# Kernel tuning notes

Measured on AMD Instinct MI355X. Metric: run time of the kernel, lower is better.

Reference implementation:

```python
import jax, jax.numpy as jnp
import numpy as np

N_NODES = 50000
N_EDGES = 800000
NODE_DIM = 8
EDGE_DIM = 3
HIDDEN = 256
EMBED = 256
HEADS = 4
HEAD_DIM = HIDDEN // HEADS
LAYERS = 3
NUM_GRAPHS = 64
NEG_SLOPE = 0.2


def layer_norm(x, g, b, eps=1e-5):
    mu = jnp.mean(x, axis=-1, keepdims=True)
    var = jnp.var(x, axis=-1, keepdims=True)
    return (x - mu) * jax.lax.rsqrt(var + eps) * g + b


def setup_inputs() -> dict:
    key = jax.random.key(0)
    ks = jax.random.split(key, 20)
    s = lambda d: 1.0 / np.sqrt(d)
    inp = {
        "x": jax.random.normal(ks[0], (N_NODES, NODE_DIM), jnp.float32),
        "edge_index": jax.random.randint(ks[1], (2, N_EDGES), 0, N_NODES, jnp.int64),
        "edge_attr": jax.random.normal(ks[2], (N_EDGES, EDGE_DIM), jnp.float32),
        "batch": jnp.sort(jax.random.randint(ks[3], (N_NODES,), 0, NUM_GRAPHS, jnp.int64)),
        # input projection + LayerNorm
        "W_in": jax.random.normal(ks[4], (NODE_DIM, HIDDEN), jnp.float32) * s(NODE_DIM),
        "b_in": jnp.zeros((HIDDEN,), jnp.float32),
        "ln_in_g": jnp.ones((HIDDEN,), jnp.float32),
        "ln_in_b": jnp.zeros((HIDDEN,), jnp.float32),
        # stacked GAT layer params [LAYERS, ...]
        "W_gat": jax.random.normal(ks[5], (LAYERS, HIDDEN, HIDDEN), jnp.float32) * s(HIDDEN),
        "b_gat": jnp.zeros((LAYERS, HIDDEN), jnp.float32),
        "W_e": jax.random.normal(ks[6], (LAYERS, EDGE_DIM, HIDDEN), jnp.float32) * s(EDGE_DIM),
        "a_src": jax.random.normal(ks[7], (LAYERS, HEADS, HEAD_DIM), jnp.float32) * s(HEAD_DIM),
        "a_dst": jax.random.normal(ks[8], (LAYERS, HEADS, HEAD_DIM), jnp.float32) * s(HEAD_DIM),
        "a_edge": jax.random.normal(ks[9], (LAYERS, HEADS, HEAD_DIM), jnp.float32) * s(HEAD_DIM),
        # output projection + LayerNorm
        "W_out": jax.random.normal(ks[10], (EMBED, EMBED), jnp.float32) * s(EMBED),
        "b_out": jnp.zeros((EMBED,), jnp.float32),
        "ln_out_g": jnp.ones((EMBED,), jnp.float32),
        "ln_out_b": jnp.zeros((EMBED,), jnp.float32),
    }
    return inp


def gat_layer(h, src, dst, edge_attr, W, b, We, a_s, a_d, a_e):
    N = h.shape[0]
    hp = (h @ W + b).reshape(N, HEADS, HEAD_DIM)                 # [N,H,D]
    ep = (edge_attr @ We).reshape(-1, HEADS, HEAD_DIM)           # [E,H,D]
    hs = hp[src]                                                 # [E,H,D] gather
    hd = hp[dst]
    logit = (hs * a_s).sum(-1) + (hd * a_d).sum(-1) + (ep * a_e).sum(-1)  # [E,H]
    logit = jax.nn.leaky_relu(logit, NEG_SLOPE)
    # segment softmax over incoming edges per destination node
    m = jax.ops.segment_max(logit, dst, num_segments=N)          # [N,H]
    m = jnp.where(jnp.isfinite(m), m, 0.0)
    ex = jnp.exp(logit - m[dst])
    denom = jax.ops.segment_sum(ex, dst, num_segments=N)         # [N,H]
    alpha = ex / jnp.maximum(denom[dst], 1e-16)                  # [E,H]
    msg = hs * alpha[:, :, None]                                 # [E,H,D]
    out = jax.ops.segment_sum(msg, dst, num_segments=N).reshape(N, HIDDEN)
    return jax.nn.elu(out + h)                                   # residual + activation


def reference(x, edge_index, edge_attr, batch, W_in, b_in, ln_in_g, ln_in_b,
              W_gat, b_gat, W_e, a_src, a_dst, a_edge,
              W_out, b_out, ln_out_g, ln_out_b):
    src, dst = edge_index[0], edge_index[1]
    h = jax.nn.elu(layer_norm(x @ W_in + b_in, ln_in_g, ln_in_b))
    for l in range(LAYERS):
        h = gat_layer(h, src, dst, edge_attr,
                      W_gat[l], b_gat[l], W_e[l], a_src[l], a_dst[l], a_edge[l])
    node_emb = jax.nn.elu(layer_norm(h @ W_out + b_out, ln_out_g, ln_out_b))
    # global mean pool per graph
    sums = jax.ops.segment_sum(node_emb, batch, num_segments=NUM_GRAPHS)
    cnt = jax.ops.segment_sum(jnp.ones((node_emb.shape[0],), node_emb.dtype), batch,
                              num_segments=NUM_GRAPHS)
    graph_emb = sums / jnp.maximum(cnt, 1.0)[:, None]
    return graph_emb, node_emb
```

## Files before the change

### kernel.cpp

```cpp
#include <hip/hip_runtime.h>
#include <math.h>

#define HIDDEN 256
#define HEADS 4
#define HEAD_DIM 64
#define LAYERS 3
#define NUM_GRAPHS 64
#define NEG_SLOPE 0.2f

typedef short short8 __attribute__((ext_vector_type(8)));
typedef float floatx4 __attribute__((ext_vector_type(4)));

static __device__ __forceinline__ float elu_f(float x) {
    return x > 0.f ? x : expm1f(x);
}

static __device__ __forceinline__ float waveReduceSum(float v) {
#pragma unroll
    for (int off = 32; off > 0; off >>= 1) v += __shfl_xor(v, off, 64);
    return v;
}

static __device__ __forceinline__ ushort f2bf(float f) {
    unsigned u = __float_as_uint(f);
    unsigned r = (u + 0x7FFFu + ((u >> 16) & 1u)) >> 16;
    return (ushort)r;
}
static __device__ __forceinline__ float bf2f(ushort h) {
    return __uint_as_float(((unsigned)h) << 16);
}

__global__ void hist_kernel(const int* __restrict__ dst, int* __restrict__ deg, int E) {
    int e = blockIdx.x * blockDim.x + threadIdx.x;
    if (e < E) atomicAdd(&deg[dst[e]], 1);
}

__global__ __launch_bounds__(256) void blocksum_kernel(const int* __restrict__ deg,
                                                       int* __restrict__ bsum, int N) {
    int i = blockIdx.x * 256 + threadIdx.x;
    int v = (i < N) ? deg[i] : 0;
    __shared__ int red[4];
    int s = v;
#pragma unroll
    for (int off = 32; off > 0; off >>= 1) s += __shfl_xor(s, off, 64);
    if ((threadIdx.x & 63) == 0) red[threadIdx.x >> 6] = s;
    __syncthreads();
    if (threadIdx.x == 0) bsum[blockIdx.x] = red[0] + red[1] + red[2] + red[3];
}

__global__ __launch_bounds__(256) void scan_bsums(int* __restrict__ bsum, int nblk) {
    __shared__ int sh[256];
    int t = threadIdx.x;
    int v = (t < nblk) ? bsum[t] : 0;
    sh[t] = v;
    __syncthreads();
#pragma unroll
    for (int off = 1; off < 256; off <<= 1) {
        int add = (t >= off) ? sh[t - off] : 0;
        __syncthreads();
        sh[t] += add;
        __syncthreads();
    }
    if (t < nblk) bsum[t] = sh[t] - v;
}

__global__ __launch_bounds__(256) void writeptr_kernel(const int* __restrict__ deg,
                                                       const int* __restrict__ bsum,
                                                       int* __restrict__ rowptr,
                                                       int* __restrict__ nxt,
                                                       int N, int E) {
    __shared__ int sh[256];
    int t = threadIdx.x;
    int i = blockIdx.x * 256 + t;
    int v = (i < N) ? deg[i] : 0;
    sh[t] = v;
    __syncthreads();
#pragma unroll
    for (int off = 1; off < 256; off <<= 1) {
        int add = (t >= off) ? sh[t - off] : 0;
        __syncthreads();
        sh[t] += add;
        __syncthreads();
    }
    if (i < N) {
        int r = bsum[blockIdx.x] + sh[t] - v;
        rowptr[i] = r;
        nxt[i] = r;
    }
    if (i == 0) rowptr[N] = E;
}

__global__ void scatter_kernel(const int* __restrict__ src, const int* __restrict__ dst,
                               const float* __restrict__ ea,
                               int* __restrict__ nxt, uint4* __restrict__ emeta, int E) {
    int e = blockIdx.x * blockDim.x + threadIdx.x;
    if (e >= E) return;
    int d = dst[e];
    int slot = atomicAdd(&nxt[d], 1);
    uint4 mt;
    mt.x = (unsigned)src[e];
    mt.y = __float_as_uint(ea[(size_t)e * 3]);
    mt.z = __float_as_uint(ea[(size_t)e * 3 + 1]);
    mt.w = __float_as_uint(ea[(size_t)e * 3 + 2]);
    emeta[slot] = mt;
}

__global__ void wea_kernel(const float* __restrict__ We, const float* __restrict__ a_e,
                           float* __restrict__ w_ea) {
    int t = threadIdx.x;
    if (t < LAYERS * HEADS * 3) {
        int l = t / 12, r = t % 12, h = r / 3, k = r % 3;
        float s = 0.f;
        for (int d = 0; d < HEAD_DIM; ++d)
            s += We[l * 3 * HIDDEN + k * HIDDEN + h * HEAD_DIM + d] *
                 a_e[l * HIDDEN + h * HEAD_DIM + d];
        w_ea[t] = s;
    }
}

__global__ void conv_w(const float* __restrict__ Wg, const float* __restrict__ Wo,
                       ushort* __restrict__ Wt) {
    int l = blockIdx.x;
    int n = blockIdx.y;
    int k = threadIdx.x;
    const float* W = (l < 3) ? (Wg + (size_t)l * HIDDEN * HIDDEN) : Wo;
    Wt[(size_t)l * HIDDEN * HIDDEN + (size_t)n * HIDDEN + k] =
        f2bf(W[(size_t)k * HIDDEN + n]);
}

__global__ __launch_bounds__(256) void inproj_ln(const float* __restrict__ x,
                                                 const float* __restrict__ W,
                                                 const float* __restrict__ b,
                                                 const float* __restrict__ g,
                                                 const float* __restrict__ beta,
                                                 float* __restrict__ h,
                                                 ushort* __restrict__ hb) {
    int n = blockIdx.x;
    int c = threadIdx.x;
    float acc = b[c];
#pragma unroll
    for (int k = 0; k < 8; ++k) acc += x[n * 8 + k] * W[k * HIDDEN + c];
    __shared__ float red[8];
    float s = waveReduceSum(acc);
    float s2 = waveReduceSum(acc * acc);
    int w = c >> 6;
    if ((c & 63) == 0) { red[w] = s; red[4 + w] = s2; }
    __syncthreads();
    float mu = (red[0] + red[1] + red[2] + red[3]) * (1.f / 256.f);
    float ms = (red[4] + red[5] + red[6] + red[7]) * (1.f / 256.f);
    float inv = rsqrtf(ms - mu * mu + 1e-5f);
    float y = elu_f((acc - mu) * inv * g[c] + beta[c]);
    h[(size_t)n * HIDDEN + c] = y;
    hb[(size_t)n * HIDDEN + c] = f2bf(y);
}

__global__ __launch_bounds__(256) void ln_elu(const float* __restrict__ t,
                                              const float* __restrict__ g,
                                              const float* __restrict__ beta,
                                              float* __restrict__ out) {
    int n = blockIdx.x;
    int c = threadIdx.x;
    float acc = t[(size_t)n * HIDDEN + c];
    __shared__ float red[8];
    float s = waveReduceSum(acc);
    float s2 = waveReduceSum(acc * acc);
    int w = c >> 6;
    if ((c & 63) == 0) { red[w] = s; red[4 + w] = s2; }
    __syncthreads();
    float mu = (red[0] + red[1] + red[2] + red[3]) * (1.f / 256.f);
    float ms = (red[4] + red[5] + red[6] + red[7]) * (1.f / 256.f);
    float inv = rsqrtf(ms - mu * mu + 1e-5f);
    float y = (acc - mu) * inv * g[c] + beta[c];
    out[(size_t)n * HIDDEN + c] = elu_f(y);
}

#define ASTR 40
__global__ __launch_bounds__(256) void gemm_mfma(const ushort* __restrict__ A,
                                                 const ushort* __restrict__ Bt,
                                                 const float* __restrict__ bias,
                                                 float* __restrict__ C32,
                                                 ushort* __restrict__ C16,
                                                 const float* __restrict__ a_s,
                                                 const float* __restrict__ a_d,
                                                 float* __restrict__ s_src,
                                                 float* __restrict__ s_dst,
                                                 int doScore) {
    const int K = 256;
    __shared__ ushort As[128 * ASTR];
    __shared__ ushort Bs[128 * ASTR];
    int m0 = blockIdx.x * 128;
    int n0 = blockIdx.y * 128;
    int t = threadIdx.x;
    int wave = t >> 6, lane = t & 63;
    int wr = wave >> 1, wc = wave & 1;
    int lrow = lane & 15;
    int quad = lane >> 4;
    floatx4 acc[4][4] = {};
    int r = t >> 2, q = t & 3;
    const ushort* Ar0 = A + (size_t)(m0 + r) * K + q * 8;
    const ushort* Ar1 = A + (size_t)(m0 + r + 64) * K + q * 8;
    const ushort* Br0 = Bt + (size_t)(n0 + r) * K + q * 8;
    const ushort* Br1 = Bt + (size_t)(n0 + r + 64) * K + q * 8;
    uint4 ra0 = *(const uint4*)(Ar0);
    uint4 ra1 = *(const uint4*)(Ar1);
    uint4 rb0 = *(const uint4*)(Br0);
    uint4 rb1 = *(const uint4*)(Br1);
    for (int k0 = 0; k0 < K; k0 += 32) {
        *(uint4*)&As[(r) * ASTR + q * 8] = ra0;
        *(uint4*)&As[(r + 64) * ASTR + q * 8] = ra1;
        *(uint4*)&Bs[(r) * ASTR + q * 8] = rb0;
        *(uint4*)&Bs[(r + 64) * ASTR + q * 8] = rb1;
        __syncthreads();
        if (k0 + 32 < K) {
            ra0 = *(const uint4*)(Ar0 + k0 + 32);
            ra1 = *(const uint4*)(Ar1 + k0 + 32);
            rb0 = *(const uint4*)(Br0 + k0 + 32);
            rb1 = *(const uint4*)(Br1 + k0 + 32);
        }
        short8 af[4], bfr[4];
#pragma unroll
        for (int i = 0; i < 4; ++i)
            af[i] = *(const short8*)&As[(wr * 64 + i * 16 + lrow) * ASTR + quad * 8];
#pragma unroll
        for (int j = 0; j < 4; ++j)
            bfr[j] = *(const short8*)&Bs[(wc * 64 + j * 16 + lrow) * ASTR + quad * 8];
#pragma unroll
        for (int i = 0; i < 4; ++i)
#pragma unroll
            for (int j = 0; j < 4; ++j)
                acc[i][j] = __builtin_amdgcn_mfma_f32_16x16x32_bf16(af[i], bfr[j],
                                                                    acc[i][j], 0, 0, 0);
        __syncthreads();
    }
    int hh = (n0 + wc * 64) >> 6;
    int ncol[4];
    float bv4[4], asv[4], adv[4];
#pragma unroll
    for (int j = 0; j < 4; ++j) {
        int n = n0 + wc * 64 + j * 16 + lrow;
        ncol[j] = n;
        bv4[j] = bias[n];
        asv[j] = a_s[n];
        adv[j] = a_d[n];
    }
#pragma unroll
    for (int i = 0; i < 4; ++i) {
#pragma unroll
        for (int rg = 0; rg < 4; ++rg) {
            int mrow = m0 + wr * 64 + i * 16 + quad * 4 + rg;
            float ps = 0.f, pd = 0.f;
#pragma unroll
            for (int j = 0; j < 4; ++j) {
                float v = acc[i][j][rg] + bv4[j];
                if (C32) C32[(size_t)mrow * HIDDEN + ncol[j]] = v;
                if (C16) C16[(size_t)mrow * HIDDEN + ncol[j]] = f2bf(v);
                ps = fmaf(v, asv[j], ps);
                pd = fmaf(v, adv[j], pd);
            }
            if (doScore) {
#pragma unroll
                for (int off = 1; off < 16; off <<= 1) {
                    ps += __shfl_xor(ps, off, 64);
                    pd += __shfl_xor(pd, off, 64);
                }
                if (lrow == 0) {
                    s_src[mrow * 4 + hh] = ps;
                    s_dst[mrow * 4 + hh] = pd;
                }
            }
        }
    }
}

__global__ __launch_bounds__(256) void aggregate(const int* __restrict__ rowptr,
                                                 const uint4* __restrict__ emeta,
                                                 const float* __restrict__ wea_l,
                                                 const float* __restrict__ s_src,
                                                 const float* __restrict__ s_dst,
                                                 const ushort* __restrict__ hpb,
                                                 const float* __restrict__ h_in,
                                                 float* __restrict__ h_out,
                                                 ushort* __restrict__ h_out_bf,
                                                 int N) {
    int wv = threadIdx.x >> 6;
    int n = blockIdx.x * 4 + wv;
    if (n >= N) return;
    int l = threadIdx.x & 63;
    int h = l >> 4;
    int e4 = l & 15;
    int c0 = l * 4;
    float w0 = wea_l[h * 3], w1 = wea_l[h * 3 + 1], w2 = wea_l[h * 3 + 2];
    float sdn = s_dst[n * 4 + h];
    int beg = rowptr[n];
    int cnt = rowptr[n + 1] - beg;
    float m = -3e38f, dsum = 0.f, a0 = 0.f, a1 = 0.f, a2 = 0.f, a3 = 0.f;
    for (int ch = 0; ch < cnt; ch += 16) {
        int i = ch + e4;
        int s = 0;
        float lg = -3e38f;
        if (i < cnt) {
            uint4 mt = emeta[beg + i];
            s = (int)mt.x;
            float esc = __uint_as_float(mt.y) * w0 + __uint_as_float(mt.z) * w1 +
                        __uint_as_float(mt.w) * w2;
            float tv = sdn + s_src[s * 4 + h] + esc;
            lg = tv > 0.f ? tv : NEG_SLOPE * tv;
        }
        float cm = lg;
#pragma unroll
        for (int off = 1; off < 16; off <<= 1)
            cm = fmaxf(cm, __shfl_xor(cm, off, 64));
        float mn = fmaxf(m, cm);
        float scl = __expf(m - mn);
        m = mn;
        dsum *= scl; a0 *= scl; a1 *= scl; a2 *= scl; a3 *= scl;
        float ex = __expf(lg - mn);
        int lim = min(16, cnt - ch);
#pragma unroll 4
        for (int j = 0; j < lim; ++j) {
            float exj = __shfl(ex, (h << 4) | j, 64);
            int sj = __shfl(s, j, 64);
            uint2 v = *(const uint2*)(hpb + (size_t)sj * HIDDEN + c0);
            dsum += exj;
            float f0 = __uint_as_float(v.x << 16);
            float f1 = __uint_as_float(v.x & 0xFFFF0000u);
            float f2 = __uint_as_float(v.y << 16);
            float f3 = __uint_as_float(v.y & 0xFFFF0000u);
            a0 = fmaf(f0, exj, a0);
            a1 = fmaf(f1, exj, a1);
            a2 = fmaf(f2, exj, a2);
            a3 = fmaf(f3, exj, a3);
        }
    }
    float inv = 1.f / fmaxf(dsum, 1e-16f);
    float4 hi = *(const float4*)(h_in + (size_t)n * HIDDEN + c0);
    float y0 = elu_f(fmaf(a0, inv, hi.x));
    float y1 = elu_f(fmaf(a1, inv, hi.y));
    float y2 = elu_f(fmaf(a2, inv, hi.z));
    float y3 = elu_f(fmaf(a3, inv, hi.w));
    float4 yo = {y0, y1, y2, y3};
    *(float4*)(h_out + (size_t)n * HIDDEN + c0) = yo;
    ushort4 yb = {f2bf(y0), f2bf(y1), f2bf(y2), f2bf(y3)};
    *(ushort4*)(h_out_bf + (size_t)n * HIDDEN + c0) = yb;
}

__global__ __launch_bounds__(256) void pool_partial(const float* __restrict__ nemb,
                                                    const int* __restrict__ batch,
                                                    float* __restrict__ gout, int N) {
    int r0 = blockIdx.x * 128;
    int c = threadIdx.x;
    __shared__ int bsh[128];
    if (c < 128) {
        int r = r0 + c;
        bsh[c] = (r < N) ? batch[r] : -1;
    }
    __syncthreads();
    int rend = min(128, N - r0);
    float acc = 0.f;
    int cur = bsh[0];
    for (int i = 0; i < rend; ++i) {
        int g = bsh[i];
        if (g != cur) {
            atomicAdd(&gout[cur * HIDDEN + c], acc);
            acc = 0.f;
            cur = g;
        }
        acc += nemb[(size_t)(r0 + i) * HIDDEN + c];
    }
    if (cur >= 0) atomicAdd(&gout[cur * HIDDEN + c], acc);
}

__global__ void pool_div(float* __restrict__ gout, const int* __restrict__ batch, int N) {
    int g = blockIdx.x;
    int c = threadIdx.x;
    int lo = 0, hi = N;
    while (lo < hi) { int mid = (lo + hi) >> 1; if (batch[mid] < g) lo = mid + 1; else hi = mid; }
    int start = lo;
    lo = start; hi = N;
    while (lo < hi) { int mid = (lo + hi) >> 1; if (batch[mid] < g + 1) lo = mid + 1; else hi = mid; }
    float cnt = (float)(lo - start);
    gout[g * HIDDEN + c] /= fmaxf(cnt, 1.f);
}

extern "C" void kernel_launch(void* const* d_in, const int* in_sizes, int n_in,
                              void* d_out, int out_size, void* d_ws, size_t ws_size,
                              hipStream_t stream) {
    const float* x       = (const float*)d_in[0];
    const int*   ei      = (const int*)d_in[1];
    const float* ea      = (const float*)d_in[2];
    const int*   batch   = (const int*)d_in[3];
    const float* W_in    = (const float*)d_in[4];
    const float* b_in    = (const float*)d_in[5];
    const float* ln_in_g = (const float*)d_in[6];
    const float* ln_in_b = (const float*)d_in[7];
    const float* W_gat   = (const float*)d_in[8];
    const float* b_gat   = (const float*)d_in[9];
    const float* W_e     = (const float*)d_in[10];
    const float* a_src   = (const float*)d_in[11];
    const float* a_dst   = (const float*)d_in[12];
    const float* a_edge  = (const float*)d_in[13];
    const float* W_out   = (const float*)d_in[14];
    const float* b_out   = (const float*)d_in[15];
    const float* ln_out_g= (const float*)d_in[16];
    const float* ln_out_b= (const float*)d_in[17];

    int N = in_sizes[0] / 8;
    int E = in_sizes[1] / 2;
    int Mpad = (N + 127) & ~127;
    int nblk = (N + 255) / 256;
    const int* srcA = ei;
    const int* dstA = ei + E;

    char* w = (char*)d_ws;
    size_t off = 0;
    auto alloc = [&](size_t bytes) {
        void* p = w + off;
        off += (bytes + 255) & ~(size_t)255;
        return p;
    };
    float*    hA     = (float*)alloc((size_t)Mpad * HIDDEN * 4);
    float*    hB     = (float*)alloc((size_t)Mpad * HIDDEN * 4);
    ushort*   hAb    = (ushort*)alloc((size_t)Mpad * HIDDEN * 2);
    ushort*   hBb    = (ushort*)alloc((size_t)Mpad * HIDDEN * 2);
    ushort*   hpb    = (ushort*)alloc((size_t)Mpad * HIDDEN * 2);
    float*    sSrc   = (float*)alloc((size_t)Mpad * 4 * 4);
    float*    sDst   = (float*)alloc((size_t)Mpad * 4 * 4);
    int*      deg    = (int*)alloc((size_t)N * 4);
    int*      rowptr = (int*)alloc((size_t)(N + 1) * 4);
    int*      nxt    = (int*)alloc((size_t)N * 4);
    int*      bsum   = (int*)alloc(256 * 4);
    uint4*    emeta  = (uint4*)alloc((size_t)E * 16);
    float*    wea    = (float*)alloc(64 * 4);
    ushort*   Wt     = (ushort*)alloc((size_t)4 * HIDDEN * HIDDEN * 2);

    hipMemsetAsync(deg, 0, (size_t)N * 4, stream);
    hist_kernel<<<(E + 255) / 256, 256, 0, stream>>>(dstA, deg, E);
    blocksum_kernel<<<nblk, 256, 0, stream>>>(deg, bsum, N);
    scan_bsums<<<1, 256, 0, stream>>>(bsum, nblk);
    writeptr_kernel<<<nblk, 256, 0, stream>>>(deg, bsum, rowptr, nxt, N, E);
    wea_kernel<<<1, 64, 0, stream>>>(W_e, a_edge, wea);
    scatter_kernel<<<(E + 255) / 256, 256, 0, stream>>>(srcA, dstA, ea, nxt, emeta, E);
    conv_w<<<dim3(4, HIDDEN), 256, 0, stream>>>(W_gat, W_out, Wt);

    inproj_ln<<<N, 256, 0, stream>>>(x, W_in, b_in, ln_in_g, ln_in_b, hA, hAb);

    float* hcur = hA;   ushort* hcurb = hAb;
    float* hnext = hB;  ushort* hnextb = hBb;
    dim3 gg(Mpad / 128, HIDDEN / 128);
    for (int l = 0; l < LAYERS; ++l) {
        gemm_mfma<<<gg, 256, 0, stream>>>(hcurb, Wt + (size_t)l * HIDDEN * HIDDEN,
                                          b_gat + l * HIDDEN, nullptr, hpb,
                                          a_src + l * HIDDEN, a_dst + l * HIDDEN,
                                          sSrc, sDst, 1);
        aggregate<<<(N + 3) / 4, 256, 0, stream>>>(rowptr, emeta, wea + l * 12,
                                                   sSrc, sDst, hpb, hcur, hnext,
                                                   hnextb, N);
        float* tf = hcur; hcur = hnext; hnext = tf;
        ushort* tb = hcurb; hcurb = hnextb; hnextb = tb;
    }

    float* hp32 = hnext;
    gemm_mfma<<<gg, 256, 0, stream>>>(hcurb, Wt + (size_t)3 * HIDDEN * HIDDEN,
                                      b_out, hp32, nullptr, a_src, a_dst, sSrc, sDst, 0);
    float* gout = (float*)d_out;
    float* nemb = gout + (size_t)NUM_GRAPHS * HIDDEN;
    ln_elu<<<N, 256, 0, stream>>>(hp32, ln_out_g, ln_out_b, nemb);
    hipMemsetAsync(gout, 0, (size_t)NUM_GRAPHS * HIDDEN * 4, stream);
    pool_partial<<<(N + 127) / 128, 256, 0, stream>>>(nemb, batch, gout, N);
    pool_div<<<NUM_GRAPHS, 256, 0, stream>>>(gout, batch, N);
}
```

Measured before the change: 688.0 us.

## Drop fp32 hidden-state copies and batch neighbor gathers in aggregate

Removes the fp32 copy of the hidden state. The residual path now reads the bf16 copy, which cuts fp32 writes from inproj and aggregate and the fp32 residual read. The aggregate loop is restructured so that full 16-edge chunks are unrolled: all shuffles are done first and all 16 gathers are issued before any FMA, giving more memory-level parallelism. The trade-offs are higher register pressure and lower residual precision, since the residual is rounded to bf16 every layer.

```diff
diff --git a/kernel.cpp b/kernel.cpp
--- a/kernel.cpp
+++ b/kernel.cpp
@@ -133,7 +133,6 @@
                                                  const float* __restrict__ b,
                                                  const float* __restrict__ g,
                                                  const float* __restrict__ beta,
-                                                 float* __restrict__ h,
                                                  ushort* __restrict__ hb) {
     int n = blockIdx.x;
     int c = threadIdx.x;
@@ -150,7 +149,6 @@
     float ms = (red[4] + red[5] + red[6] + red[7]) * (1.f / 256.f);
     float inv = rsqrtf(ms - mu * mu + 1e-5f);
     float y = elu_f((acc - mu) * inv * g[c] + beta[c]);
-    h[(size_t)n * HIDDEN + c] = y;
     hb[(size_t)n * HIDDEN + c] = f2bf(y);
 }
 
@@ -278,8 +276,7 @@
                                                  const float* __restrict__ s_src,
                                                  const float* __restrict__ s_dst,
                                                  const ushort* __restrict__ hpb,
-                                                 const float* __restrict__ h_in,
-                                                 float* __restrict__ h_out,
+                                                 const ushort* __restrict__ h_in_bf,
                                                  ushort* __restrict__ h_out_bf,
                                                  int N) {
     int wv = threadIdx.x >> 6;
@@ -294,7 +291,44 @@
     int beg = rowptr[n];
     int cnt = rowptr[n + 1] - beg;
     float m = -3e38f, dsum = 0.f, a0 = 0.f, a1 = 0.f, a2 = 0.f, a3 = 0.f;
-    for (int ch = 0; ch < cnt; ch += 16) {
+    int ch = 0;
+    for (; ch + 16 <= cnt; ch += 16) {
+        uint4 mt = emeta[beg + ch + e4];
+        int s = (int)mt.x;
+        float esc = __uint_as_float(mt.y) * w0 + __uint_as_float(mt.z) * w1 +
+                    __uint_as_float(mt.w) * w2;
+        float tv = sdn + s_src[s * 4 + h] + esc;
+        float lg = tv > 0.f ? tv : NEG_SLOPE * tv;
+        float cm = lg;
+#pragma unroll
+        for (int off = 1; off < 16; off <<= 1)
+            cm = fmaxf(cm, __shfl_xor(cm, off, 64));
+        float mn = fmaxf(m, cm);
+        float scl = __expf(m - mn);
+        m = mn;
+        dsum *= scl; a0 *= scl; a1 *= scl; a2 *= scl; a3 *= scl;
+        float ex = __expf(lg - mn);
+        float exj[16];
+        int sj[16];
+#pragma unroll
+        for (int j = 0; j < 16; ++j) {
+            exj[j] = __shfl(ex, (h << 4) | j, 64);
+            sj[j] = __shfl(s, j, 64);
+        }
+        uint2 v[16];
+#pragma unroll
+        for (int j = 0; j < 16; ++j)
+            v[j] = *(const uint2*)(hpb + (size_t)sj[j] * HIDDEN + c0);
+#pragma unroll
+        for (int j = 0; j < 16; ++j) {
+            dsum += exj[j];
+            a0 = fmaf(__uint_as_float(v[j].x << 16), exj[j], a0);
+            a1 = fmaf(__uint_as_float(v[j].x & 0xFFFF0000u), exj[j], a1);
+            a2 = fmaf(__uint_as_float(v[j].y << 16), exj[j], a2);
+            a3 = fmaf(__uint_as_float(v[j].y & 0xFFFF0000u), exj[j], a3);
+        }
+    }
+    if (ch < cnt) {
         int i = ch + e4;
         int s = 0;
         float lg = -3e38f;
@@ -315,31 +349,25 @@
         m = mn;
         dsum *= scl; a0 *= scl; a1 *= scl; a2 *= scl; a3 *= scl;
         float ex = __expf(lg - mn);
-        int lim = min(16, cnt - ch);
+        int lim = cnt - ch;
 #pragma unroll 4
         for (int j = 0; j < lim; ++j) {
             float exj = __shfl(ex, (h << 4) | j, 64);
             int sj = __shfl(s, j, 64);
             uint2 v = *(const uint2*)(hpb + (size_t)sj * HIDDEN + c0);
             dsum += exj;
-            float f0 = __uint_as_float(v.x << 16);
-            float f1 = __uint_as_float(v.x & 0xFFFF0000u);
-            float f2 = __uint_as_float(v.y << 16);
-            float f3 = __uint_as_float(v.y & 0xFFFF0000u);
-            a0 = fmaf(f0, exj, a0);
-            a1 = fmaf(f1, exj, a1);
-            a2 = fmaf(f2, exj, a2);
-            a3 = fmaf(f3, exj, a3);
+            a0 = fmaf(__uint_as_float(v.x << 16), exj, a0);
+            a1 = fmaf(__uint_as_float(v.x & 0xFFFF0000u), exj, a1);
+            a2 = fmaf(__uint_as_float(v.y << 16), exj, a2);
+            a3 = fmaf(__uint_as_float(v.y & 0xFFFF0000u), exj, a3);
         }
     }
     float inv = 1.f / fmaxf(dsum, 1e-16f);
-    float4 hi = *(const float4*)(h_in + (size_t)n * HIDDEN + c0);
-    float y0 = elu_f(fmaf(a0, inv, hi.x));
-    float y1 = elu_f(fmaf(a1, inv, hi.y));
-    float y2 = elu_f(fmaf(a2, inv, hi.z));
-    float y3 = elu_f(fmaf(a3, inv, hi.w));
-    float4 yo = {y0, y1, y2, y3};
-    *(float4*)(h_out + (size_t)n * HIDDEN + c0) = yo;
+    ushort4 hib = *(const ushort4*)(h_in_bf + (size_t)n * HIDDEN + c0);
+    float y0 = elu_f(fmaf(a0, inv, bf2f(hib.x)));
+    float y1 = elu_f(fmaf(a1, inv, bf2f(hib.y)));
+    float y2 = elu_f(fmaf(a2, inv, bf2f(hib.z)));
+    float y3 = elu_f(fmaf(a3, inv, bf2f(hib.w)));
     ushort4 yb = {f2bf(y0), f2bf(y1), f2bf(y2), f2bf(y3)};
     *(ushort4*)(h_out_bf + (size_t)n * HIDDEN + c0) = yb;
 }
@@ -418,11 +446,10 @@
         off += (bytes + 255) & ~(size_t)255;
         return p;
     };
-    float*    hA     = (float*)alloc((size_t)Mpad * HIDDEN * 4);
-    float*    hB     = (float*)alloc((size_t)Mpad * HIDDEN * 4);
     ushort*   hAb    = (ushort*)alloc((size_t)Mpad * HIDDEN * 2);
     ushort*   hBb    = (ushort*)alloc((size_t)Mpad * HIDDEN * 2);
     ushort*   hpb    = (ushort*)alloc((size_t)Mpad * HIDDEN * 2);
+    float*    hp32   = (float*)alloc((size_t)Mpad * HIDDEN * 4);
     float*    sSrc   = (float*)alloc((size_t)Mpad * 4 * 4);
     float*    sDst   = (float*)alloc((size_t)Mpad * 4 * 4);
     int*      deg    = (int*)alloc((size_t)N * 4);
@@ -442,10 +469,10 @@
     scatter_kernel<<<(E + 255) / 256, 256, 0, stream>>>(srcA, dstA, ea, nxt, emeta, E);
     conv_w<<<dim3(4, HIDDEN), 256, 0, stream>>>(W_gat, W_out, Wt);
 
-    inproj_ln<<<N, 256, 0, stream>>>(x, W_in, b_in, ln_in_g, ln_in_b, hA, hAb);
-
-    float* hcur = hA;   ushort* hcurb = hAb;
-    float* hnext = hB;  ushort* hnextb = hBb;
+    inproj_ln<<<N, 256, 0, stream>>>(x, W_in, b_in, ln_in_g, ln_in_b, hAb);
+
+    ushort* hcurb = hAb;
+    ushort* hnextb = hBb;
     dim3 gg(Mpad / 128, HIDDEN / 128);
     for (int l = 0; l < LAYERS; ++l) {
         gemm_mfma<<<gg, 256, 0, stream>>>(hcurb, Wt + (size_t)l * HIDDEN * HIDDEN,
@@ -453,13 +480,10 @@
                                           a_src + l * HIDDEN, a_dst + l * HIDDEN,
                                           sSrc, sDst, 1);
         aggregate<<<(N + 3) / 4, 256, 0, stream>>>(rowptr, emeta, wea + l * 12,
-                                                   sSrc, sDst, hpb, hcur, hnext,
-                                                   hnextb, N);
-        float* tf = hcur; hcur = hnext; hnext = tf;
+                                                   sSrc, sDst, hpb, hcurb, hnextb, N);
         ushort* tb = hcurb; hcurb = hnextb; hnextb = tb;
     }
 
-    float* hp32 = hnext;
     gemm_mfma<<<gg, 256, 0, stream>>>(hcurb, Wt + (size_t)3 * HIDDEN * HIDDEN,
                                       b_out, hp32, nullptr, a_src, a_dst, sSrc, sDst, 0);
     float* gout = (float*)d_out;
```

After: 717.6 us. +4.3%, slower.
